# Kernel optimization log

Measured on AMD Instinct MI355X. Metric: run time of the kernel, lower is better.

## Reference

```python
import jax, jax.numpy as jnp
import numpy as np
from jax import lax

N, C1, C2, H, W = 4, 256, 256, 80, 80
CH = 128           # c_ = int(c2 * e)
G, KS = 1, 3       # groups, kernel_size
K = KS * KS        # sampling points per group
PAD, DIL = 1, 1
EPS_BN, EPS_LN = 1e-5, 1e-6


def conv_bn_silu(x, w, g, b, m, v, stride=1):
    # ultralytics Conv: conv(bias=False) + BatchNorm2d(eval) + SiLU
    pad = (w.shape[2] - 1) // 2
    y = lax.conv_general_dilated(x, w, (stride, stride), [(pad, pad), (pad, pad)],
                                 dimension_numbers=('NCHW', 'OIHW', 'NCHW'))
    s = g / jnp.sqrt(v + EPS_BN)
    y = y * s[None, :, None, None] + (b - m * s)[None, :, None, None]
    return jax.nn.silu(y)


def dcnv3_core(x, offset, mask):
    # x: (N,H,W,C) NHWC; offset: (N,H,W,G*K*2); mask: (N,H,W,G,K) softmaxed over K
    n, h, w, c = x.shape
    gc = c // G
    xp = jnp.pad(x, ((0, 0), (PAD, PAD), (PAD, PAD), (0, 0)))
    Hp, Wp = h + 2 * PAD, w + 2 * PAD
    base = (DIL * (KS - 1)) // 2
    # reference points (normalized by padded spatial size), stride 1
    ref_x = (jnp.arange(w, dtype=x.dtype) + base + 0.5) / Wp   # (W,)
    ref_y = (jnp.arange(h, dtype=x.dtype) + base + 0.5) / Hp   # (H,)
    gx = (jnp.arange(KS, dtype=x.dtype) * DIL - base) / Wp
    gy = (jnp.arange(KS, dtype=x.dtype) * DIL - base) / Hp
    grid_x = jnp.repeat(gx, KS)   # point p = i*KS + j -> x = gx[i]
    grid_y = jnp.tile(gy, KS)     # y = gy[j]  (torch meshgrid 'ij' ordering)
    off = offset.reshape(n, h, w, G, K, 2)
    loc_x = ref_x[None, None, :, None, None] + grid_x + off[..., 0] / Wp
    loc_y = ref_y[None, :, None, None, None] + grid_y + off[..., 1] / Hp
    # grid_sample align_corners=False: pixel = norm * size - 0.5
    px = loc_x * Wp - 0.5
    py = loc_y * Hp - 0.5
    x0 = jnp.floor(px); y0 = jnp.floor(py)
    lw, lh = px - x0, py - y0
    x0i, y0i = x0.astype(jnp.int32), y0.astype(jnp.int32)
    xv = jnp.transpose(xp.reshape(n, Hp * Wp, G, gc), (0, 2, 1, 3))  # (N,G,S,gc)
    tw = lambda a: jnp.transpose(a, (0, 3, 1, 2, 4))[..., None]      # (N,H,W,G,K)->(N,G,H,W,K,1)

    def gather(yi, xi):
        valid = ((xi >= 0) & (xi < Wp) & (yi >= 0) & (yi < Hp)).astype(x.dtype)
        idx = jnp.clip(yi, 0, Hp - 1) * Wp + jnp.clip(xi, 0, Wp - 1)
        idx = jnp.transpose(idx, (0, 3, 1, 2, 4)).reshape(n, G, h * w * K)
        v = jnp.take_along_axis(xv, idx[..., None], axis=2).reshape(n, G, h, w, K, gc)
        return v * tw(valid)   # zeros padding_mode

    out = (gather(y0i, x0i) * tw((1 - lh) * (1 - lw))
           + gather(y0i, x0i + 1) * tw((1 - lh) * lw)
           + gather(y0i + 1, x0i) * tw(lh * (1 - lw))
           + gather(y0i + 1, x0i + 1) * tw(lh * lw))   # (N,G,H,W,K,gc)
    m = jnp.transpose(mask, (0, 3, 1, 2, 4))[..., None]
    out = (out * m).sum(axis=4)                        # (N,G,H,W,gc)
    return jnp.transpose(out, (0, 2, 3, 1, 4)).reshape(n, h, w, c)


def forward(x, w1, g1, b1, m1, v1, w2, g2, b2, m2, v2,
            dw_w, dw_b, ln_g, ln_b, off_w, off_b, msk_w, msk_b,
            in_w, in_b, out_w, out_b, g3, b3, m3, v3):
    y = conv_bn_silu(x, w1, g1, b1, m1, v1)   # cv1: 3x3 Conv c1->c_
    y = conv_bn_silu(y, w2, g2, b2, m2, v2)   # cv2.conv: 1x1 Conv c_->c2
    t = jnp.transpose(y, (0, 2, 3, 1))        # NHWC
    x_proj = t @ in_w.T + in_b                # input_proj
    # dw_conv: depthwise 3x3 -> LayerNorm (channels_last) -> GELU
    dw = lax.conv_general_dilated(y, dw_w, (1, 1), [(1, 1), (1, 1)],
                                  dimension_numbers=('NCHW', 'OIHW', 'NCHW'),
                                  feature_group_count=C2)
    dw = jnp.transpose(dw, (0, 2, 3, 1)) + dw_b
    mu = dw.mean(-1, keepdims=True)
    var = ((dw - mu) ** 2).mean(-1, keepdims=True)
    dw = (dw - mu) / jnp.sqrt(var + EPS_LN) * ln_g + ln_b
    dw = jax.nn.gelu(dw, approximate=False)
    offset = dw @ off_w.T + off_b                                       # (N,H,W,G*K*2)
    mask = jax.nn.softmax((dw @ msk_w.T + msk_b).reshape(N, H, W, G, K), axis=-1)
    z = dcnv3_core(x_proj, offset, mask)
    z = z @ out_w.T + out_b                   # output_proj
    z = jnp.transpose(z, (0, 3, 1, 2))        # NCHW
    s = g3 / jnp.sqrt(v3 + EPS_BN)
    z = z * s[None, :, None, None] + (b3 - m3 * s)[None, :, None, None]
    z = jax.nn.silu(z)
    return x + z                              # shortcut (c1 == c2)


def setup_inputs():
    key = jax.random.key(0)
    ks = jax.random.split(key, 16)
    r = lambda k, s, sc=0.05: jax.random.normal(k, s, dtype=jnp.float32) * sc
    return {
        'x': jax.random.normal(ks[0], (N, C1, H, W), dtype=jnp.float32),
        'w1': r(ks[1], (CH, C1, 3, 3)),
        'g1': jnp.ones((CH,), jnp.float32), 'b1': jnp.zeros((CH,), jnp.float32),
        'm1': r(ks[2], (CH,), 0.1),
        'v1': jax.random.uniform(ks[3], (CH,), jnp.float32, 0.5, 1.5),
        'w2': r(ks[4], (C2, CH, 1, 1)),
        'g2': jnp.ones((C2,), jnp.float32), 'b2': jnp.zeros((C2,), jnp.float32),
        'm2': r(ks[5], (C2,), 0.1),
        'v2': jax.random.uniform(ks[6], (C2,), jnp.float32, 0.5, 1.5),
        'dw_w': r(ks[7], (C2, 1, 3, 3)), 'dw_b': jnp.zeros((C2,), jnp.float32),
        'ln_g': jnp.ones((C2,), jnp.float32), 'ln_b': jnp.zeros((C2,), jnp.float32),
        'off_w': r(ks[8], (G * K * 2, C2), 0.01), 'off_b': jnp.zeros((G * K * 2,), jnp.float32),
        'msk_w': r(ks[9], (G * K, C2), 0.01), 'msk_b': jnp.zeros((G * K,), jnp.float32),
        'in_w': r(ks[10], (C2, C2)), 'in_b': jnp.zeros((C2,), jnp.float32),
        'out_w': r(ks[11], (C2, C2)), 'out_b': jnp.zeros((C2,), jnp.float32),
        'g3': jnp.ones((C2,), jnp.float32), 'b3': jnp.zeros((C2,), jnp.float32),
        'm3': r(ks[12], (C2,), 0.1),
        'v3': jax.random.uniform(ks[13], (C2,), jnp.float32, 0.5, 1.5),
    }


def reference(x, w1, g1, b1, m1, v1, w2, g2, b2, m2, v2,
              dw_w, dw_b, ln_g, ln_b, off_w, off_b, msk_w, msk_b,
              in_w, in_b, out_w, out_b, g3, b3, m3, v3):
    return forward(x, w1, g1, b1, m1, v1, w2, g2, b2, m2, v2,
                   dw_w, dw_b, ln_g, ln_b, off_w, off_b, msk_w, msk_b,
                   in_w, in_b, out_w, out_b, g3, b3, m3, v3)
```

## Files before the change

kernel.cpp:

```cpp
#include <hip/hip_runtime.h>
#include <cmath>

#define TN 4
#define TC1 256
#define TCH 128
#define TC2 256
#define TH 80
#define TW 80
#define THP 82
#define TWP 84
#define NPIX (TN*TH*TW)

#define OFF_WBF   0
#define OFF_W2B   294912
#define OFF_INWB  327680
#define OFF_OUTWB 393216
#define OFF_DWT   458752
#define OFF_WCAT  461056
#define OFF_WCATB 467968
#define OFF_T1    468128
#define OFF_T2    468512
#define OFF_T3P   469024
#define OFF_XPAD  469504
#define OFF_Y1B   3997696
#define OFF_Y2N   7525888
#define OFF_RAWN  10802688
#define OFF_ZN    11493888

typedef __attribute__((ext_vector_type(8))) short bf16x8;
typedef __attribute__((ext_vector_type(4))) float f32x4;

__device__ __forceinline__ float siluf(float v) { return v / (1.f + expf(-v)); }
__device__ __forceinline__ short rnbf(float f) {
  unsigned u = __float_as_uint(f);
  unsigned r = (u + 0x7fffu + ((u >> 16) & 1u)) >> 16;
  return (short)r;
}
__device__ __forceinline__ float bf2f(short s) {
  return __uint_as_float(((unsigned)(unsigned short)s) << 16);
}

__global__ __launch_bounds__(256) void k_prep(
    const float* __restrict__ w1, const float* __restrict__ g1, const float* __restrict__ b1,
    const float* __restrict__ m1, const float* __restrict__ v1,
    const float* __restrict__ w2, const float* __restrict__ g2, const float* __restrict__ b2,
    const float* __restrict__ m2, const float* __restrict__ v2,
    const float* __restrict__ dww, const float* __restrict__ offw, const float* __restrict__ offb,
    const float* __restrict__ mskw, const float* __restrict__ mskb,
    const float* __restrict__ inw, const float* __restrict__ outw, const float* __restrict__ outb,
    const float* __restrict__ g3, const float* __restrict__ b3,
    const float* __restrict__ m3, const float* __restrict__ v3,
    const float* __restrict__ x, float* __restrict__ ws)
{
  __shared__ short lds[80 * 40];
  if (blockIdx.x >= 1836) {
    short* xpn = (short*)(ws + OFF_XPAD);
    int b = blockIdx.x - 1836;
    int cc = b & 7; int hp = (b >> 3) % THP; int n = b / (THP * 8);
    int c0 = cc * 32;
    int t = threadIdx.x;
    int h = hp - 1;
    bool hv = (h >= 0 && h < TH);
    if (hv) {
      for (int f = t; f < 640; f += 256) {
        int ci = f / 20; int w4 = (f - ci * 20) * 4;
        float4 xv = *(const float4*)(x + ((n * TC1 + c0 + ci) * TH + h) * TW + w4);
        lds[(w4 + 0) * 40 + ci] = rnbf(xv.x);
        lds[(w4 + 1) * 40 + ci] = rnbf(xv.y);
        lds[(w4 + 2) * 40 + ci] = rnbf(xv.z);
        lds[(w4 + 3) * 40 + ci] = rnbf(xv.w);
      }
    }
    __syncthreads();
    short* op = xpn + ((n * THP + hp) * TWP) * TC2 + c0;
    for (int g = t; g < 672; g += 256) {
      int ci4 = (g & 7) * 4; int wp = g >> 3;
      short4 v = {0, 0, 0, 0};
      if (hv && wp >= 1 && wp <= TW) v = *(const short4*)(&lds[(wp - 1) * 40 + ci4]);
      *(short4*)(op + wp * TC2 + ci4) = v;
    }
    return;
  }
  int i = blockIdx.x * 256 + threadIdx.x;
  if (i < 294912) {
    int co = i / 2304; int r = i - co * 2304;
    int tap = r >> 8; int ci = r & 255; int ky = tap / 3; int kx = tap - ky * 3;
    float s = g1[co] * __frsqrt_rn(v1[co] + 1e-5f);
    ((short*)(ws + OFF_WBF))[i] = rnbf(w1[((co * TC1 + ci) * 3 + ky) * 3 + kx] * s);
    return;
  }
  i -= 294912;
  if (i < 32768) {
    int co = i >> 7; int ci = i & 127;
    float s = g2[co] * __frsqrt_rn(v2[co] + 1e-5f);
    ((short*)(ws + OFF_W2B))[i] = rnbf(w2[co * TCH + ci] * s);
    return;
  }
  i -= 32768;
  if (i < 65536) {
    int co = i >> 8; int ci = i & 255;
    ((short*)(ws + OFF_INWB))[i] = rnbf(inw[co * TC2 + ci]);
    return;
  }
  i -= 65536;
  if (i < 65536) {
    int co = i >> 8; int ci = i & 255;
    float s = g3[co] * __frsqrt_rn(v3[co] + 1e-5f);
    ((short*)(ws + OFF_OUTWB))[i] = rnbf(outw[co * TC2 + ci] * s);
    return;
  }
  i -= 65536;
  if (i < 2304) { int c = i & 255; int j = i >> 8; ws[OFF_DWT + i] = dww[c * 9 + j]; return; }
  i -= 2304;
  if (i < 8192) {
    int c = i & 255; int j = i >> 8;
    float v = 0.f;
    if (j < 18) v = offw[j * 256 + c];
    else if (j < 27) v = mskw[(j - 18) * 256 + c];
    ((short*)(ws + OFF_WCAT))[i] = rnbf(v);
    return;
  }
  i -= 8192;
  if (i < 27) { ws[OFF_WCATB + i] = (i < 18) ? offb[i] : mskb[i - 18]; return; }
  i -= 27;
  if (i < 128) { float s = g1[i] / sqrtf(v1[i] + 1e-5f); ws[OFF_T1 + i] = b1[i] - m1[i] * s; return; }
  i -= 128;
  if (i < 256) { float s = g2[i] / sqrtf(v2[i] + 1e-5f); ws[OFF_T2 + i] = b2[i] - m2[i] * s; return; }
  i -= 256;
  if (i < 256) { float s = g3[i] / sqrtf(v3[i] + 1e-5f); ws[OFF_T3P + i] = outb[i] * s + b3[i] - m3[i] * s; return; }
}

#define BH_STR 40
#define BH_PIX 108
__global__ __launch_bounds__(256) void k_cv1f(const short* __restrict__ xpn, const short* __restrict__ wbf,
                                              const float* __restrict__ t1v, short* __restrict__ y1b)
{
  __shared__ short Bh[2][BH_PIX * BH_STR];

  int b = blockIdx.x;
  int wt = b % 5; b /= 5; int ht = b % 20; int n = b / 20;
  int w0 = wt * 16, h0 = ht * 4;

  int tid = threadIdx.x;
  int wave = tid >> 6, lane = tid & 63;
  int ln = lane & 15, q = lane >> 4;
  int co0 = wave * 32;

  int u0 = tid, u1 = tid + 256;
  int p0 = u0 >> 2, s0 = u0 & 3;
  int p1 = u1 >> 2, s1 = u1 & 3;
  int hh0 = p0 / 18, ww0 = p0 - hh0 * 18;
  int hh1 = p1 / 18, ww1 = p1 - hh1 * 18;
  const short* sb0 = xpn + ((n * THP + h0 + hh0) * TWP + (w0 + ww0)) * 256 + s0 * 8;
  const short* sb1 = xpn + ((n * THP + h0 + hh1) * TWP + (w0 + ww1)) * 256 + s1 * 8;
  bool hasu1 = (u1 < 432);
  int d0 = p0 * BH_STR + s0 * 8;
  int d1 = p1 * BH_STR + s1 * 8;

  const short* abase = wbf + (co0 + ln) * 2304 + q * 8;

  f32x4 acc[2][4];
#pragma unroll
  for (int i = 0; i < 2; ++i)
#pragma unroll
    for (int j = 0; j < 4; ++j) acc[i][j] = (f32x4){0.f, 0.f, 0.f, 0.f};

  bf16x8 rb0 = *(const bf16x8*)(sb0);
  bf16x8 rb1 = {0, 0, 0, 0, 0, 0, 0, 0};
  if (hasu1) rb1 = *(const bf16x8*)(sb1);
  *(bf16x8*)(&Bh[0][d0]) = rb0;
  if (hasu1) *(bf16x8*)(&Bh[0][d1]) = rb1;
  __syncthreads();

  for (int cc = 0; cc < 8; ++cc) {
    int cur = cc & 1;
    bf16x8 af[9][2];
#pragma unroll
    for (int tap = 0; tap < 9; ++tap)
#pragma unroll
      for (int mt = 0; mt < 2; ++mt)
        af[tap][mt] = *(const bf16x8*)(abase + (mt * 16) * 2304 + tap * 256 + cc * 32);
    if (cc < 7) {
      rb0 = *(const bf16x8*)(sb0 + (cc + 1) * 32);
      if (hasu1) rb1 = *(const bf16x8*)(sb1 + (cc + 1) * 32);
    }
#pragma unroll
    for (int tap = 0; tap < 9; ++tap) {
      const int ky = tap / 3, kx = tap - (tap / 3) * 3;
      bf16x8 bv[4];
#pragma unroll
      for (int nt = 0; nt < 4; ++nt) {
        int pr = nt * 16 + ln;
        int hr = pr >> 4, wc = pr & 15;
        bv[nt] = *(const bf16x8*)(&Bh[cur][((hr + ky) * 18 + (wc + kx)) * BH_STR + q * 8]);
      }
#pragma unroll
      for (int mt = 0; mt < 2; ++mt)
#pragma unroll
        for (int nt = 0; nt < 4; ++nt)
          acc[mt][nt] = __builtin_amdgcn_mfma_f32_16x16x32_bf16(af[tap][mt], bv[nt], acc[mt][nt], 0, 0, 0);
    }
    if (cc < 7) {
      *(bf16x8*)(&Bh[cur ^ 1][d0]) = rb0;
      if (hasu1) *(bf16x8*)(&Bh[cur ^ 1][d1]) = rb1;
      __syncthreads();
    }
  }

#pragma unroll
  for (int mt = 0; mt < 2; ++mt) {
    int co = co0 + mt * 16 + q * 4;
    float t0 = t1v[co], t1 = t1v[co + 1], t2 = t1v[co + 2], t3 = t1v[co + 3];
#pragma unroll
    for (int nt = 0; nt < 4; ++nt) {
      int pr = nt * 16 + ln;
      int hr = pr >> 4, wc = pr & 15;
      int pix = (n * TH + h0 + hr) * TW + (w0 + wc);
      short4 p;
      p.x = rnbf(siluf(acc[mt][nt][0] + t0));
      p.y = rnbf(siluf(acc[mt][nt][1] + t1));
      p.z = rnbf(siluf(acc[mt][nt][2] + t2));
      p.w = rnbf(siluf(acc[mt][nt][3] + t3));
      *(short4*)(y1b + pix * TCH + co) = p;
    }
  }
}

#define A_STR 40
__global__ __launch_bounds__(256) void k_cv2(const short* __restrict__ y1b, const short* __restrict__ w2b,
                                             const float* __restrict__ t2v, short* __restrict__ y2b)
{
  __shared__ short As[2][128 * A_STR];
  __shared__ short Bs[2][128 * A_STR];

  int b = blockIdx.x;
  int ch = b & 1; int pt = b >> 1;
  int co_base = ch * 128;
  int pix0 = pt * 128;

  int tid = threadIdx.x;
  int wave = tid >> 6, lane = tid & 63;
  int ln = lane & 15, q = lane >> 4;
  int coh = (wave & 1) * 64;
  int pxh = (wave >> 1) * 64;

  int srow = tid >> 1;
  int ssub = (tid & 1) * 16;
  const short* arow = w2b + (co_base + srow) * TCH + ssub;
  const short* brow = y1b + (pix0 + srow) * TCH + ssub;

  f32x4 acc[4][4];
#pragma unroll
  for (int i = 0; i < 4; ++i)
#pragma unroll
    for (int j = 0; j < 4; ++j) acc[i][j] = (f32x4){0.f, 0.f, 0.f, 0.f};

  bf16x8 ra0, ra1, rb0, rb1;
  auto grab = [&](int c) {
    const short* ap = arow + c * 32;
    const short* bp = brow + c * 32;
    ra0 = *(const bf16x8*)(ap);
    ra1 = *(const bf16x8*)(ap + 8);
    rb0 = *(const bf16x8*)(bp);
    rb1 = *(const bf16x8*)(bp + 8);
  };
  auto put = [&](int buf) {
    int o = srow * A_STR + ssub;
    *(bf16x8*)(&As[buf][o])     = ra0;
    *(bf16x8*)(&As[buf][o + 8]) = ra1;
    *(bf16x8*)(&Bs[buf][o])     = rb0;
    *(bf16x8*)(&Bs[buf][o + 8]) = rb1;
  };
  auto comp = [&](int buf) {
    bf16x8 af[4], bfv[4];
#pragma unroll
    for (int mt = 0; mt < 4; ++mt)
      af[mt] = *(const bf16x8*)(&As[buf][(coh + mt * 16 + ln) * A_STR + q * 8]);
#pragma unroll
    for (int nt = 0; nt < 4; ++nt)
      bfv[nt] = *(const bf16x8*)(&Bs[buf][(pxh + nt * 16 + ln) * A_STR + q * 8]);
#pragma unroll
    for (int mt = 0; mt < 4; ++mt)
#pragma unroll
      for (int nt = 0; nt < 4; ++nt)
        acc[mt][nt] = __builtin_amdgcn_mfma_f32_16x16x32_bf16(af[mt], bfv[nt], acc[mt][nt], 0, 0, 0);
  };

  const int NCH = TCH / 32;
  grab(0);
  put(0);
  __syncthreads();
  for (int c = 0; c < NCH; ++c) {
    if (c < NCH - 1) grab(c + 1);
    comp(c & 1);
    if (c < NCH - 1) {
      __syncthreads();
      put((c + 1) & 1);
      __syncthreads();
    }
  }

#pragma unroll
  for (int mt = 0; mt < 4; ++mt) {
    int co = co_base + coh + mt * 16 + q * 4;
    float t0 = t2v[co], t1 = t2v[co + 1], t2 = t2v[co + 2], t3 = t2v[co + 3];
#pragma unroll
    for (int nt = 0; nt < 4; ++nt) {
      int pix = pix0 + pxh + nt * 16 + ln;
      short4 p;
      p.x = rnbf(siluf(acc[mt][nt][0] + t0));
      p.y = rnbf(siluf(acc[mt][nt][1] + t1));
      p.z = rnbf(siluf(acc[mt][nt][2] + t2));
      p.w = rnbf(siluf(acc[mt][nt][3] + t3));
      *(short4*)(y2b + pix * TC2 + co) = p;
    }
  }
}

#define DT_STR 264
__global__ __launch_bounds__(256) void k_pidw(
    const short* __restrict__ y2b, const short* __restrict__ inwb, const float* __restrict__ inb,
    short* __restrict__ xproj,
    const float* __restrict__ dwt, const float* __restrict__ dwb, const float* __restrict__ lng,
    const float* __restrict__ lnb, const short* __restrict__ wcatb16, const float* __restrict__ wcatb,
    float* __restrict__ raw)
{
  __shared__ short smem[4 * 128 * A_STR];

  int tid = threadIdx.x;
  int wave = tid >> 6, lane = tid & 63;

  if (blockIdx.x < 400) {
    short (*As)[128 * A_STR] = (short(*)[128 * A_STR])(smem);
    short (*Bs)[128 * A_STR] = (short(*)[128 * A_STR])(smem + 2 * 128 * A_STR);

    int b = blockIdx.x;
    int ch = b & 1; int pt = b >> 1;
    int co_base = ch * 128;
    int pix0 = pt * 128;

    int ln = lane & 15, q = lane >> 4;
    int coh = (wave & 1) * 64;
    int pxh = (wave >> 1) * 64;

    int srow = tid >> 1;
    int ssub = (tid & 1) * 16;
    const short* arow = inwb + (co_base + srow) * TC2 + ssub;
    const short* brow = y2b + (pix0 + srow) * TC2 + ssub;

    f32x4 acc[4][4];
#pragma unroll
    for (int i = 0; i < 4; ++i)
#pragma unroll
      for (int j = 0; j < 4; ++j) acc[i][j] = (f32x4){0.f, 0.f, 0.f, 0.f};

    bf16x8 ra0, ra1, rb0, rb1;
    auto grab = [&](int c) {
      const short* ap = arow + c * 32;
      const short* bp = brow + c * 32;
      ra0 = *(const bf16x8*)(ap);
      ra1 = *(const bf16x8*)(ap + 8);
      rb0 = *(const bf16x8*)(bp);
      rb1 = *(const bf16x8*)(bp + 8);
    };
    auto put = [&](int buf) {
      int o = srow * A_STR + ssub;
      *(bf16x8*)(&As[buf][o])     = ra0;
      *(bf16x8*)(&As[buf][o + 8]) = ra1;
      *(bf16x8*)(&Bs[buf][o])     = rb0;
      *(bf16x8*)(&Bs[buf][o + 8]) = rb1;
    };
    auto comp = [&](int buf) {
      bf16x8 af[4], bfv[4];
#pragma unroll
      for (int mt = 0; mt < 4; ++mt)
        af[mt] = *(const bf16x8*)(&As[buf][(coh + mt * 16 + ln) * A_STR + q * 8]);
#pragma unroll
      for (int nt = 0; nt < 4; ++nt)
        bfv[nt] = *(const bf16x8*)(&Bs[buf][(pxh + nt * 16 + ln) * A_STR + q * 8]);
#pragma unroll
      for (int mt = 0; mt < 4; ++mt)
#pragma unroll
        for (int nt = 0; nt < 4; ++nt)
          acc[mt][nt] = __builtin_amdgcn_mfma_f32_16x16x32_bf16(af[mt], bfv[nt], acc[mt][nt], 0, 0, 0);
    };

    const int NCH = TC2 / 32;
    grab(0);
    put(0);
    __syncthreads();
    for (int c = 0; c < NCH; ++c) {
      if (c < NCH - 1) grab(c + 1);
      comp(c & 1);
      if (c < NCH - 1) {
        __syncthreads();
        put((c + 1) & 1);
        __syncthreads();
      }
    }

#pragma unroll
    for (int mt = 0; mt < 4; ++mt) {
      int co = co_base + coh + mt * 16 + q * 4;
      float b0 = inb[co], b1 = inb[co + 1], b2 = inb[co + 2], b3 = inb[co + 3];
#pragma unroll
      for (int nt = 0; nt < 4; ++nt) {
        int pix = pix0 + pxh + nt * 16 + ln;
        short4 p;
        p.x = rnbf(acc[mt][nt][0] + b0);
        p.y = rnbf(acc[mt][nt][1] + b1);
        p.z = rnbf(acc[mt][nt][2] + b2);
        p.w = rnbf(acc[mt][nt][3] + b3);
        *(short4*)(xproj + pix * TC2 + co) = p;
      }
    }
    return;
  }

  short* dt = smem;

  int half = lane >> 5;
  int c0 = (lane & 31) * 8;
  int pix0 = (blockIdx.x - 400) * 32;

  float4 db0 = *(const float4*)(dwb + c0);
  float4 db1 = *(const float4*)(dwb + c0 + 4);
  float4 g0 = *(const float4*)(lng + c0);
  float4 g1 = *(const float4*)(lng + c0 + 4);
  float4 lb0 = *(const float4*)(lnb + c0);
  float4 lb1 = *(const float4*)(lnb + c0 + 4);
  float gv[8] = {g0.x, g0.y, g0.z, g0.w, g1.x, g1.y, g1.z, g1.w};
  float bvv[8] = {lb0.x, lb0.y, lb0.z, lb0.w, lb1.x, lb1.y, lb1.z, lb1.w};
  const float is2 = 0.70710678118654752f;

  for (int r = 0; r < 4; ++r) {
    int pl = wave * 8 + half * 4 + r;
    int pix = pix0 + pl;
    int w = pix % TW; int h = (pix / TW) % TH; int n = pix / (TH * TW);
    float v[8] = {db0.x, db0.y, db0.z, db0.w, db1.x, db1.y, db1.z, db1.w};
#pragma unroll
    for (int dy = 0; dy < 3; ++dy) {
#pragma unroll
      for (int dx = 0; dx < 3; ++dx) {
        int hh = h + dy - 1, ww = w + dx - 1;
        bool ok = (hh >= 0) & (hh < TH) & (ww >= 0) & (ww < TW);
        int off = ok ? (((n * TH + hh) * TW + ww) * TC2 + c0) : c0;
        bf16x8 yv = *(const bf16x8*)(y2b + off);
        float m = ok ? 1.f : 0.f;
        const float* wp = dwt + (dy * 3 + dx) * TC2 + c0;
        float4 w0 = *(const float4*)(wp);
        float4 w1 = *(const float4*)(wp + 4);
        v[0] += bf2f(yv[0]) * w0.x * m;
        v[1] += bf2f(yv[1]) * w0.y * m;
        v[2] += bf2f(yv[2]) * w0.z * m;
        v[3] += bf2f(yv[3]) * w0.w * m;
        v[4] += bf2f(yv[4]) * w1.x * m;
        v[5] += bf2f(yv[5]) * w1.y * m;
        v[6] += bf2f(yv[6]) * w1.z * m;
        v[7] += bf2f(yv[7]) * w1.w * m;
      }
    }
    float sv = 0.f, sq = 0.f;
#pragma unroll
    for (int i = 0; i < 8; ++i) { sv += v[i]; sq += v[i] * v[i]; }
#pragma unroll
    for (int o = 16; o > 0; o >>= 1) { sv += __shfl_xor(sv, o); sq += __shfl_xor(sq, o); }
    float mu = sv * (1.f / 256.f);
    float var = sq * (1.f / 256.f) - mu * mu;
    float rs = 1.f / sqrtf(var + 1e-6f);
    bf16x8 o8;
#pragma unroll
    for (int i = 0; i < 8; ++i) {
      float nv = (v[i] - mu) * rs * gv[i] + bvv[i];
      o8[i] = rnbf(0.5f * nv * (1.f + erff(nv * is2)));
    }
    *(bf16x8*)(&dt[pl * DT_STR + c0]) = o8;
  }
  __syncthreads();

  int ln = lane & 15, q = lane >> 4;
  int g = wave & 1;
  int jbase = (wave >> 1) * 16;

  f32x4 acc = {0.f, 0.f, 0.f, 0.f};
  const short* ap = wcatb16 + (jbase + ln) * 256 + q * 8;
  const short* bp = &dt[(g * 16 + ln) * DT_STR + q * 8];
#pragma unroll
  for (int kk = 0; kk < 256; kk += 32) {
    bf16x8 a  = *(const bf16x8*)(ap + kk);
    bf16x8 bf = *(const bf16x8*)(bp + kk);
    acc = __builtin_amdgcn_mfma_f32_16x16x32_bf16(a, bf, acc, 0, 0, 0);
  }

  int pix = pix0 + g * 16 + ln;
#pragma unroll
  for (int r = 0; r < 4; ++r) {
    int j = jbase + q * 4 + r;
    if (j < 27) raw[pix * 27 + j] = acc[r] + wcatb[j];
  }
}

__global__ __launch_bounds__(256) void k_dcn(const short* __restrict__ xproj, const float* __restrict__ raw,
                                             short* __restrict__ z)
{
  __shared__ int2 sp[8][36];
  int tid = threadIdx.x;
  int pixbase = blockIdx.x * 8;

  for (int j = tid; j < 288; j += 256) {
    int pxl = j / 36, t = j - pxl * 36;
    int pix = pixbase + pxl;
    int w = pix % TW; int h = (pix / TW) % TH;
    const float* r = raw + pix * 27;
    int k = t >> 2, tap = t & 3;
    int tx = tap & 1, ty = tap >> 1;
    float mx = r[18];
#pragma unroll
    for (int kk = 1; kk < 9; ++kk) mx = fmaxf(mx, r[18 + kk]);
    float sum = 0.f, ek = 0.f;
#pragma unroll
    for (int kk = 0; kk < 9; ++kk) {
      float ee = expf(r[18 + kk] - mx);
      sum += ee;
      if (kk == k) ek = ee;
    }
    float mk = ek / sum;
    float px = (float)(w + k / 3) + r[2 * k];
    float py = (float)(h + k % 3) + r[2 * k + 1];
    float x0f = floorf(px), y0f = floorf(py);
    float lw = px - x0f, lh = py - y0f;
    int x0 = (int)x0f + tx, y0 = (int)y0f + ty;
    float wt = mk * (tx ? lw : 1.f - lw) * (ty ? lh : 1.f - lh);
    bool valid = (x0 >= 1) & (x0 <= TW) & (y0 >= 1) & (y0 <= TH);
    int2 pr;
    pr.x = valid ? (((y0 - 1) * TW + (x0 - 1)) * TC2) : 0;
    pr.y = valid ? __float_as_int(wt) : 0;
    sp[pxl][t] = pr;
  }
  __syncthreads();

  int wave = tid >> 6, lane = tid & 63;
  int half = lane >> 5;
  int pxl = wave * 2 + half;
  int pix = pixbase + pxl;
  int n = pix / (TH * TW);
  int c0 = (lane & 31) * 8;
  const short* xb = xproj + n * (TH * TW * TC2) + c0;

  float a[8] = {0.f, 0.f, 0.f, 0.f, 0.f, 0.f, 0.f, 0.f};
#pragma unroll
  for (int t = 0; t < 36; ++t) {
    int2 pr = sp[pxl][t];
    float wt = __int_as_float(pr.y);
    bf16x8 v = *(const bf16x8*)(xb + pr.x);
#pragma unroll
    for (int i = 0; i < 8; ++i) a[i] += wt * bf2f(v[i]);
  }
  bf16x8 o8;
#pragma unroll
  for (int i = 0; i < 8; ++i) o8[i] = rnbf(a[i]);
  *(bf16x8*)(z + pix * TC2 + c0) = o8;
}

__global__ __launch_bounds__(256) void k_proj_out(const short* __restrict__ zb, const short* __restrict__ outwb,
                                                  const float* __restrict__ t3p,
                                                  const float* __restrict__ x, float* __restrict__ out)
{
  __shared__ short As[2][128 * A_STR];
  __shared__ short Bs[2][128 * A_STR];

  int b = blockIdx.x;
  int ch = b & 1; int pt = b >> 1;
  int co_base = ch * 128;
  int pix0 = pt * 128;

  int tid = threadIdx.x;
  int wave = tid >> 6, lane = tid & 63;
  int ln = lane & 15, q = lane >> 4;
  int coh = (wave & 1) * 64;
  int pxh = (wave >> 1) * 64;

  int srow = tid >> 1;
  int ssub = (tid & 1) * 16;
  const short* arow = outwb + (co_base + srow) * TC2 + ssub;
  const short* brow = zb + (pix0 + srow) * TC2 + ssub;

  f32x4 acc[4][4];
#pragma unroll
  for (int i = 0; i < 4; ++i)
#pragma unroll
    for (int j = 0; j < 4; ++j) acc[i][j] = (f32x4){0.f, 0.f, 0.f, 0.f};

  bf16x8 ra0, ra1, rb0, rb1;
  auto grab = [&](int c) {
    const short* ap = arow + c * 32;
    const short* bp = brow + c * 32;
    ra0 = *(const bf16x8*)(ap);
    ra1 = *(const bf16x8*)(ap + 8);
    rb0 = *(const bf16x8*)(bp);
    rb1 = *(const bf16x8*)(bp + 8);
  };
  auto put = [&](int buf) {
    int o = srow * A_STR + ssub;
    *(bf16x8*)(&As[buf][o])     = ra0;
    *(bf16x8*)(&As[buf][o + 8]) = ra1;
    *(bf16x8*)(&Bs[buf][o])     = rb0;
    *(bf16x8*)(&Bs[buf][o + 8]) = rb1;
  };
  auto comp = [&](int buf) {
    bf16x8 af[4], bfv[4];
#pragma unroll
    for (int mt = 0; mt < 4; ++mt)
      af[mt] = *(const bf16x8*)(&As[buf][(coh + mt * 16 + ln) * A_STR + q * 8]);
#pragma unroll
    for (int nt = 0; nt < 4; ++nt)
      bfv[nt] = *(const bf16x8*)(&Bs[buf][(pxh + nt * 16 + ln) * A_STR + q * 8]);
#pragma unroll
    for (int mt = 0; mt < 4; ++mt)
#pragma unroll
      for (int nt = 0; nt < 4; ++nt)
        acc[mt][nt] = __builtin_amdgcn_mfma_f32_16x16x32_bf16(af[mt], bfv[nt], acc[mt][nt], 0, 0, 0);
  };

  const int NCH = TC2 / 32;
  grab(0);
  put(0);
  __syncthreads();
  for (int c = 0; c < NCH; ++c) {
    if (c < NCH - 1) grab(c + 1);
    comp(c & 1);
    if (c < NCH - 1) {
      __syncthreads();
      put((c + 1) & 1);
      __syncthreads();
    }
  }

  __syncthreads();
  float* tb = (float*)(&As[0][0]);
  float* wb = tb + wave * 1056;
  int pixw = pix0 + pxh;
  int nn = pixw / (TH * TW);
  int hw0 = pixw - nn * (TH * TW);

#pragma unroll
  for (int mt = 0; mt < 4; ++mt) {
#pragma unroll
    for (int nt = 0; nt < 4; ++nt)
#pragma unroll
      for (int r = 0; r < 4; ++r)
        wb[(q * 4 + r) * 66 + nt * 16 + ln] = acc[mt][nt][r];
    int co = co_base + coh + mt * 16;
#pragma unroll
    for (int cl = 0; cl < 16; ++cl) {
      float vv = wb[cl * 66 + lane];
      int addr = (nn * TC2 + co + cl) * (TH * TW) + hw0 + lane;
      out[addr] = x[addr] + siluf(vv + t3p[co + cl]);
    }
  }
}

extern "C" void kernel_launch(void* const* d_in, const int* in_sizes, int n_in,
                              void* d_out, int out_size, void* d_ws, size_t ws_size,
                              hipStream_t stream)
{
  const float* x    = (const float*)d_in[0];
  const float* w1   = (const float*)d_in[1];
  const float* g1   = (const float*)d_in[2];
  const float* b1   = (const float*)d_in[3];
  const float* m1   = (const float*)d_in[4];
  const float* v1   = (const float*)d_in[5];
  const float* w2   = (const float*)d_in[6];
  const float* g2   = (const float*)d_in[7];
  const float* b2   = (const float*)d_in[8];
  const float* m2   = (const float*)d_in[9];
  const float* v2   = (const float*)d_in[10];
  const float* dww  = (const float*)d_in[11];
  const float* dwb  = (const float*)d_in[12];
  const float* lng  = (const float*)d_in[13];
  const float* lnb  = (const float*)d_in[14];
  const float* offw = (const float*)d_in[15];
  const float* offb = (const float*)d_in[16];
  const float* mskw = (const float*)d_in[17];
  const float* mskb = (const float*)d_in[18];
  const float* inw  = (const float*)d_in[19];
  const float* inb  = (const float*)d_in[20];
  const float* outw = (const float*)d_in[21];
  const float* outb = (const float*)d_in[22];
  const float* g3   = (const float*)d_in[23];
  const float* b3   = (const float*)d_in[24];
  const float* m3   = (const float*)d_in[25];
  const float* v3   = (const float*)d_in[26];

  float* ws  = (float*)d_ws;
  float* out = (float*)d_out;

  short* xpn    = (short*)(ws + OFF_XPAD);
  short* wbf    = (short*)(ws + OFF_WBF);
  short* w2b    = (short*)(ws + OFF_W2B);
  short* inwb   = (short*)(ws + OFF_INWB);
  short* outwb  = (short*)(ws + OFF_OUTWB);
  short* wcat16 = (short*)(ws + OFF_WCAT);
  short* y1b    = (short*)(ws + OFF_Y1B);
  short* y2b    = (short*)(ws + OFF_Y2N);
  float* raw    = ws + OFF_RAWN;
  short* zb     = (short*)(ws + OFF_ZN);
  short* xproj  = (short*)d_out;

  hipLaunchKernelGGL(k_prep, dim3(1836 + TN * THP * 8), dim3(256), 0, stream,
                     w1, g1, b1, m1, v1, w2, g2, b2, m2, v2,
                     dww, offw, offb, mskw, mskb, inw, outw, outb, g3, b3, m3, v3, x, ws);
  hipLaunchKernelGGL(k_cv1f,     dim3(400),   dim3(256), 0, stream, xpn, wbf, ws + OFF_T1, y1b);
  hipLaunchKernelGGL(k_cv2,      dim3(400),   dim3(256), 0, stream, y1b, w2b, ws + OFF_T2, y2b);
  hipLaunchKernelGGL(k_pidw,     dim3(1200),  dim3(256), 0, stream, y2b, inwb, inb, xproj,
                     ws + OFF_DWT, dwb, lng, lnb, wcat16, ws + OFF_WCATB, raw);
  hipLaunchKernelGGL(k_dcn,      dim3(3200),  dim3(256), 0, stream, xproj, raw, zb);
  hipLaunchKernelGGL(k_proj_out, dim3(400),   dim3(256), 0, stream, zb, outwb, ws + OFF_T3P, x, out);
}
```

Baseline: 272.0 us.

## Fuse cv1 3x3 conv and cv2 1x1 conv into one kernel via LDS

Merges the cv1 conv kernel and the cv2 1x1 conv kernel into a single kernel. The 64-pixel by 128-channel y1 tile is staged in shared memory, reusing the double-buffer space, and the cv2 GEMM runs directly on it. This removes the y1 global round-trip and one launch. In exchange each block now loads the full cv2 weight matrix from global/L2 without LDS staging, and the fused kernel carries more register pressure.

```diff
diff --git a/kernel.cpp b/kernel.cpp
--- a/kernel.cpp
+++ b/kernel.cpp
@@ -22,7 +22,6 @@
 #define OFF_T2    468512
 #define OFF_T3P   469024
 #define OFF_XPAD  469504
-#define OFF_Y1B   3997696
 #define OFF_Y2N   7525888
 #define OFF_RAWN  10802688
 #define OFF_ZN    11493888
@@ -132,10 +131,14 @@
 
 #define BH_STR 40
 #define BH_PIX 108
-__global__ __launch_bounds__(256) void k_cv1f(const short* __restrict__ xpn, const short* __restrict__ wbf,
-                                              const float* __restrict__ t1v, short* __restrict__ y1b)
+#define BH_ELE (BH_PIX * BH_STR)
+#define Y1_STR 136
+__global__ __launch_bounds__(256) void k_cv12(const short* __restrict__ xpn, const short* __restrict__ wbf,
+                                              const short* __restrict__ w2b,
+                                              const float* __restrict__ t1v, const float* __restrict__ t2v,
+                                              short* __restrict__ y2b)
 {
-  __shared__ short Bh[2][BH_PIX * BH_STR];
+  __shared__ short U[64 * Y1_STR];
 
   int b = blockIdx.x;
   int wt = b % 5; b /= 5; int ht = b % 20; int n = b / 20;
@@ -168,8 +171,8 @@
   bf16x8 rb0 = *(const bf16x8*)(sb0);
   bf16x8 rb1 = {0, 0, 0, 0, 0, 0, 0, 0};
   if (hasu1) rb1 = *(const bf16x8*)(sb1);
-  *(bf16x8*)(&Bh[0][d0]) = rb0;
-  if (hasu1) *(bf16x8*)(&Bh[0][d1]) = rb1;
+  *(bf16x8*)(&U[d0]) = rb0;
+  if (hasu1) *(bf16x8*)(&U[d1]) = rb1;
   __syncthreads();
 
   for (int cc = 0; cc < 8; ++cc) {
@@ -192,7 +195,7 @@
       for (int nt = 0; nt < 4; ++nt) {
         int pr = nt * 16 + ln;
         int hr = pr >> 4, wc = pr & 15;
-        bv[nt] = *(const bf16x8*)(&Bh[cur][((hr + ky) * 18 + (wc + kx)) * BH_STR + q * 8]);
+        bv[nt] = *(const bf16x8*)(&U[cur * BH_ELE + ((hr + ky) * 18 + (wc + kx)) * BH_STR + q * 8]);
       }
 #pragma unroll
       for (int mt = 0; mt < 2; ++mt)
@@ -201,122 +204,75 @@
           acc[mt][nt] = __builtin_amdgcn_mfma_f32_16x16x32_bf16(af[tap][mt], bv[nt], acc[mt][nt], 0, 0, 0);
     }
     if (cc < 7) {
-      *(bf16x8*)(&Bh[cur ^ 1][d0]) = rb0;
-      if (hasu1) *(bf16x8*)(&Bh[cur ^ 1][d1]) = rb1;
+      *(bf16x8*)(&U[(cur ^ 1) * BH_ELE + d0]) = rb0;
+      if (hasu1) *(bf16x8*)(&U[(cur ^ 1) * BH_ELE + d1]) = rb1;
       __syncthreads();
     }
   }
 
+  __syncthreads();
 #pragma unroll
   for (int mt = 0; mt < 2; ++mt) {
     int co = co0 + mt * 16 + q * 4;
     float t0 = t1v[co], t1 = t1v[co + 1], t2 = t1v[co + 2], t3 = t1v[co + 3];
+#pragma unroll
+    for (int nt = 0; nt < 4; ++nt) {
+      int px = nt * 16 + ln;
+      short4 p;
+      p.x = rnbf(siluf(acc[mt][nt][0] + t0));
+      p.y = rnbf(siluf(acc[mt][nt][1] + t1));
+      p.z = rnbf(siluf(acc[mt][nt][2] + t2));
+      p.w = rnbf(siluf(acc[mt][nt][3] + t3));
+      *(short4*)(&U[px * Y1_STR + co]) = p;
+    }
+  }
+  __syncthreads();
+
+  int coh2 = wave * 64;
+  const short* a2base = w2b + (coh2 + ln) * TCH + q * 8;
+
+  f32x4 acc2[4][4];
+#pragma unroll
+  for (int i = 0; i < 4; ++i)
+#pragma unroll
+    for (int j = 0; j < 4; ++j) acc2[i][j] = (f32x4){0.f, 0.f, 0.f, 0.f};
+
+#pragma unroll
+  for (int c = 0; c < 4; ++c) {
+    bf16x8 a2[4], b2[4];
+#pragma unroll
+    for (int mt = 0; mt < 4; ++mt)
+      a2[mt] = *(const bf16x8*)(a2base + (mt * 16) * TCH + c * 32);
+#pragma unroll
+    for (int nt = 0; nt < 4; ++nt)
+      b2[nt] = *(const bf16x8*)(&U[(nt * 16 + ln) * Y1_STR + c * 32 + q * 8]);
+#pragma unroll
+    for (int mt = 0; mt < 4; ++mt)
+#pragma unroll
+      for (int nt = 0; nt < 4; ++nt)
+        acc2[mt][nt] = __builtin_amdgcn_mfma_f32_16x16x32_bf16(a2[mt], b2[nt], acc2[mt][nt], 0, 0, 0);
+  }
+
+#pragma unroll
+  for (int mt = 0; mt < 4; ++mt) {
+    int co = coh2 + mt * 16 + q * 4;
+    float t0 = t2v[co], t1 = t2v[co + 1], t2 = t2v[co + 2], t3 = t2v[co + 3];
 #pragma unroll
     for (int nt = 0; nt < 4; ++nt) {
       int pr = nt * 16 + ln;
       int hr = pr >> 4, wc = pr & 15;
       int pix = (n * TH + h0 + hr) * TW + (w0 + wc);
       short4 p;
-      p.x = rnbf(siluf(acc[mt][nt][0] + t0));
-      p.y = rnbf(siluf(acc[mt][nt][1] + t1));
-      p.z = rnbf(siluf(acc[mt][nt][2] + t2));
-      p.w = rnbf(siluf(acc[mt][nt][3] + t3));
-      *(short4*)(y1b + pix * TCH + co) = p;
+      p.x = rnbf(siluf(acc2[mt][nt][0] + t0));
+      p.y = rnbf(siluf(acc2[mt][nt][1] + t1));
+      p.z = rnbf(siluf(acc2[mt][nt][2] + t2));
+      p.w = rnbf(siluf(acc2[mt][nt][3] + t3));
+      *(short4*)(y2b + pix * TC2 + co) = p;
     }
   }
 }
 
 #define A_STR 40
-__global__ __launch_bounds__(256) void k_cv2(const short* __restrict__ y1b, const short* __restrict__ w2b,
-                                             const float* __restrict__ t2v, short* __restrict__ y2b)
-{
-  __shared__ short As[2][128 * A_STR];
-  __shared__ short Bs[2][128 * A_STR];
-
-  int b = blockIdx.x;
-  int ch = b & 1; int pt = b >> 1;
-  int co_base = ch * 128;
-  int pix0 = pt * 128;
-
-  int tid = threadIdx.x;
-  int wave = tid >> 6, lane = tid & 63;
-  int ln = lane & 15, q = lane >> 4;
-  int coh = (wave & 1) * 64;
-  int pxh = (wave >> 1) * 64;
-
-  int srow = tid >> 1;
-  int ssub = (tid & 1) * 16;
-  const short* arow = w2b + (co_base + srow) * TCH + ssub;
-  const short* brow = y1b + (pix0 + srow) * TCH + ssub;
-
-  f32x4 acc[4][4];
-#pragma unroll
-  for (int i = 0; i < 4; ++i)
-#pragma unroll
-    for (int j = 0; j < 4; ++j) acc[i][j] = (f32x4){0.f, 0.f, 0.f, 0.f};
-
-  bf16x8 ra0, ra1, rb0, rb1;
-  auto grab = [&](int c) {
-    const short* ap = arow + c * 32;
-    const short* bp = brow + c * 32;
-    ra0 = *(const bf16x8*)(ap);
-    ra1 = *(const bf16x8*)(ap + 8);
-    rb0 = *(const bf16x8*)(bp);
-    rb1 = *(const bf16x8*)(bp + 8);
-  };
-  auto put = [&](int buf) {
-    int o = srow * A_STR + ssub;
-    *(bf16x8*)(&As[buf][o])     = ra0;
-    *(bf16x8*)(&As[buf][o + 8]) = ra1;
-    *(bf16x8*)(&Bs[buf][o])     = rb0;
-    *(bf16x8*)(&Bs[buf][o + 8]) = rb1;
-  };
-  auto comp = [&](int buf) {
-    bf16x8 af[4], bfv[4];
-#pragma unroll
-    for (int mt = 0; mt < 4; ++mt)
-      af[mt] = *(const bf16x8*)(&As[buf][(coh + mt * 16 + ln) * A_STR + q * 8]);
-#pragma unroll
-    for (int nt = 0; nt < 4; ++nt)
-      bfv[nt] = *(const bf16x8*)(&Bs[buf][(pxh + nt * 16 + ln) * A_STR + q * 8]);
-#pragma unroll
-    for (int mt = 0; mt < 4; ++mt)
-#pragma unroll
-      for (int nt = 0; nt < 4; ++nt)
-        acc[mt][nt] = __builtin_amdgcn_mfma_f32_16x16x32_bf16(af[mt], bfv[nt], acc[mt][nt], 0, 0, 0);
-  };
-
-  const int NCH = TCH / 32;
-  grab(0);
-  put(0);
-  __syncthreads();
-  for (int c = 0; c < NCH; ++c) {
-    if (c < NCH - 1) grab(c + 1);
-    comp(c & 1);
-    if (c < NCH - 1) {
-      __syncthreads();
-      put((c + 1) & 1);
-      __syncthreads();
-    }
-  }
-
-#pragma unroll
-  for (int mt = 0; mt < 4; ++mt) {
-    int co = co_base + coh + mt * 16 + q * 4;
-    float t0 = t2v[co], t1 = t2v[co + 1], t2 = t2v[co + 2], t3 = t2v[co + 3];
-#pragma unroll
-    for (int nt = 0; nt < 4; ++nt) {
-      int pix = pix0 + pxh + nt * 16 + ln;
-      short4 p;
-      p.x = rnbf(siluf(acc[mt][nt][0] + t0));
-      p.y = rnbf(siluf(acc[mt][nt][1] + t1));
-      p.z = rnbf(siluf(acc[mt][nt][2] + t2));
-      p.w = rnbf(siluf(acc[mt][nt][3] + t3));
-      *(short4*)(y2b + pix * TC2 + co) = p;
-    }
-  }
-}
-
 #define DT_STR 264
 __global__ __launch_bounds__(256) void k_pidw(
     const short* __restrict__ y2b, const short* __restrict__ inwb, const float* __restrict__ inb,
@@ -701,7 +657,6 @@
   short* inwb   = (short*)(ws + OFF_INWB);
   short* outwb  = (short*)(ws + OFF_OUTWB);
   short* wcat16 = (short*)(ws + OFF_WCAT);
-  short* y1b    = (short*)(ws + OFF_Y1B);
   short* y2b    = (short*)(ws + OFF_Y2N);
   float* raw    = ws + OFF_RAWN;
   short* zb     = (short*)(ws + OFF_ZN);
@@ -710,8 +665,8 @@
   hipLaunchKernelGGL(k_prep, dim3(1836 + TN * THP * 8), dim3(256), 0, stream,
                      w1, g1, b1, m1, v1, w2, g2, b2, m2, v2,
                      dww, offw, offb, mskw, mskb, inw, outw, outb, g3, b3, m3, v3, x, ws);
-  hipLaunchKernelGGL(k_cv1f,     dim3(400),   dim3(256), 0, stream, xpn, wbf, ws + OFF_T1, y1b);
-  hipLaunchKernelGGL(k_cv2,      dim3(400),   dim3(256), 0, stream, y1b, w2b, ws + OFF_T2, y2b);
+  hipLaunchKernelGGL(k_cv12,     dim3(400),   dim3(256), 0, stream, xpn, wbf, w2b,
+                     ws + OFF_T1, ws + OFF_T2, y2b);
   hipLaunchKernelGGL(k_pidw,     dim3(1200),  dim3(256), 0, stream, y2b, inwb, inb, xproj,
                      ws + OFF_DWT, dwb, lng, lnb, wcat16, ws + OFF_WCATB, raw);
   hipLaunchKernelGGL(k_dcn,      dim3(3200),  dim3(256), 0, stream, xproj, raw, zb);
```

New measurement: 269.0 us, median of 2. No clear change (-1.1%).
